# Performance work log

Measured on AMD Instinct MI355X. Metric: run time of the kernel, lower is better.

## Reference

```python
import jax, jax.numpy as jnp
import numpy as np

B, NO, NM, NV, E = 16, 512, 128, 64, 256
H, DK, MS, FF = 16, 16, 8, 512
TRANS_MAX = 100.0


def _ln(x):
    m = x.mean(-1, keepdims=True)
    v = ((x - m) ** 2).mean(-1, keepdims=True)
    return (x - m) * jax.lax.rsqrt(v + 1e-5)


def _inv_norm(x):
    # 1 - minmax-normalize over the whole per-batch matrix
    mn = x.min(axis=(1, 2), keepdims=True)
    mx = x.max(axis=(1, 2), keepdims=True)
    return 1.0 - (x - mn) / (mx - mn)


def _adjacency(proc_time, trans_time, MVpair_trans, mask_dyn, mask_ma):
    # masked copy of proc_time
    A_proc = jnp.where(mask_dyn, proc_time, 0.0)
    # keep only the per-row minimum nonzero entry (min_ProcTime_elements)
    nz = jnp.where(A_proc == 0.0, jnp.inf, A_proc)
    mn = nz.min(axis=2, keepdims=True)
    keep = (A_proc == mn) & (A_proc != 0.0)
    A_proc = A_proc * keep.astype(proc_time.dtype)
    A_proc_norm = (A_proc > 0.0).astype(proc_time.dtype)
    # machine-machine masks
    mask2 = mask_ma[:, None, :] & mask_ma[:, :, None]  # [B, nm, nm]
    A_procing = (~mask2).astype(proc_time.dtype)
    A_off = _inv_norm(MVpair_trans)
    tt = jnp.where(mask2, trans_time, TRANS_MAX + 1.0)
    A_on = _inv_norm(tt)
    return A_proc_norm, A_procing, A_off, A_on


def _block(row, col, cost, Wq, Wk, Wv, Wo, mW1, mb1, mW2, mb2, fW1, fb1, fW2, fb2):
    # MatNet-style mixed-score multi-head attention encoding block
    Bb, R, _ = row.shape
    C = col.shape[1]
    q = (row @ Wq).reshape(Bb, R, H, DK).transpose(0, 2, 1, 3)  # bhrd
    k = (col @ Wk).reshape(Bb, C, H, DK).transpose(0, 2, 1, 3)  # bhcd
    v = (col @ Wv).reshape(Bb, C, H, DK).transpose(0, 2, 1, 3)
    dot = jnp.einsum('bhrd,bhcd->bhrc', q, k) / jnp.sqrt(jnp.asarray(DK, row.dtype))
    two = jnp.stack([dot, jnp.broadcast_to(cost[:, None], dot.shape)], axis=-1)  # [B,H,R,C,2]
    hmix = jax.nn.relu(jnp.einsum('bhrct,hts->bhrcs', two, mW1) + mb1[None, :, None, None, :])
    score = jnp.einsum('bhrcs,hso->bhrco', hmix, mW2)[..., 0] + mb2[:, 0][None, :, None, None]
    attn = jax.nn.softmax(score, axis=-1)
    ctx = jnp.einsum('bhrc,bhcd->bhrd', attn, v).transpose(0, 2, 1, 3).reshape(Bb, R, H * DK)
    out1 = _ln(row + ctx @ Wo)
    ffn = jax.nn.relu(out1 @ fW1 + fb1) @ fW2 + fb2
    return _ln(out1 + ffn)


def setup_inputs() -> dict:
    key = jax.random.key(0)
    ks = jax.random.split(key, 24)

    def nrm(i, shape, s=0.05):
        return jax.random.normal(ks[i], shape, jnp.float32) * s

    return {
        'ope_emb': nrm(0, (B, NO, E), 1.0),
        'ma_emb': nrm(1, (B, NM, E), 1.0),
        'veh_emb': nrm(2, (B, NV, E), 1.0),
        'proc_time': jax.random.uniform(ks[3], (B, NO, NM), jnp.float32) * 20.0,
        'offload_trans_time': jax.random.uniform(ks[4], (B, NO, NV), jnp.float32) * TRANS_MAX,
        'trans_time': jax.random.uniform(ks[5], (B, NM, NM), jnp.float32) * TRANS_MAX,
        'MVpair_trans': jax.random.uniform(ks[6], (B, NV, NM), jnp.float32) * TRANS_MAX,
        'mask_dyn_ope_ma_adj': jax.random.bernoulli(ks[7], 0.3, (B, NO, NM)),
        'mask_ma': jax.random.bernoulli(ks[8], 0.7, (B, NM)),
        # stacked params for the 4 blocks: 0=ope, 1=veh, 2=ma1, 3=ma2
        'Wq': nrm(9, (4, E, H * DK)),
        'Wk': nrm(10, (4, E, H * DK)),
        'Wv': nrm(11, (4, E, H * DK)),
        'Wo': nrm(12, (4, H * DK, E)),
        'mixW1': nrm(13, (4, H, 2, MS), 0.3),
        'mixb1': jnp.zeros((4, H, MS), jnp.float32),
        'mixW2': nrm(14, (4, H, MS, 1), 0.3),
        'mixb2': jnp.zeros((4, H, 1), jnp.float32),
        'ffW1': nrm(15, (4, E, FF)),
        'ffb1': jnp.zeros((4, FF), jnp.float32),
        'ffW2': nrm(16, (4, FF, E)),
        'ffb2': jnp.zeros((4, E), jnp.float32),
        'maprojW': nrm(17, (2 * E, E)),
        'maprojb': jnp.zeros((E,), jnp.float32),
    }


def reference(ope_emb, ma_emb, veh_emb, proc_time, offload_trans_time, trans_time,
              MVpair_trans, mask_dyn_ope_ma_adj, mask_ma,
              Wq, Wk, Wv, Wo, mixW1, mixb1, mixW2, mixb2,
              ffW1, ffb1, ffW2, ffb2, maprojW, maprojb):
    A_proc_norm, A_procing, A_off, A_on = _adjacency(
        proc_time, trans_time, MVpair_trans, mask_dyn_ope_ma_adj, mask_ma)

    def blk(i, row, col, cost):
        return _block(row, col, cost, Wq[i], Wk[i], Wv[i], Wo[i],
                      mixW1[i], mixb1[i], mixW2[i], mixb2[i],
                      ffW1[i], ffb1[i], ffW2[i], ffb2[i])

    ope_out = blk(0, ope_emb, ma_emb, A_proc_norm)
    veh_out = blk(1, veh_emb, ma_emb, A_off)
    ma1 = blk(2, ma_emb, ma_emb, A_procing)
    ma2 = blk(3, ma_emb, ma_emb, A_on)
    ma_out = jnp.concatenate([ma1, ma2], axis=-1) @ maprojW + maprojb
    return (ope_out, ma_out, veh_out)
```

## Files before the change

kernel.cpp:

```cpp
#include <hip/hip_runtime.h>
#include <hip/hip_fp16.h>
#include <hip/hip_bf16.h>


typedef unsigned short u16;
typedef __attribute__((ext_vector_type(8))) short bf16x8;
typedef __attribute__((ext_vector_type(4))) float f32x4;
struct us4 { u16 x, y, z, w; };

__device__ __forceinline__ float bf2f(u16 u) {
  return __uint_as_float(((unsigned int)u) << 16);
}
__device__ __forceinline__ u16 f2bf(float f) {
  unsigned int x = __float_as_uint(f);
  x += 0x7FFFu + ((x >> 16) & 1u);
  return (u16)(x >> 16);
}
__device__ __forceinline__ __half2 h2max(__half2 a, __half2 b) {
  unsigned au = *(unsigned*)&a, bu = *(unsigned*)&b, ru;
  asm("v_pk_max_f16 %0, %1, %2" : "=v"(ru) : "v"(au), "v"(bu));
  return *(__half2*)&ru;
}

#define NBATCH 16
#define NOPE   512
#define NMA    128
#define NVEH   64
#define EDIM   256

struct PrepArgs {
  const float* ope; const float* ma; const float* veh;
  u16* ope_bf; u16* ma_bf; u16* veh_bf;
  const float* proc; const int* mask_dyn; float* A_proc;
  const float* mv; const float* trans; const int* mask_ma;
  unsigned int* mm;
};
struct TrArgs {
  const float* Wq; const float* Wk; const float* Wv; const float* Wo;
  const float* ffW1; const float* ffW2; const float* maproj;
  u16* WqT; u16* WkT; u16* WvT; u16* WoT; u16* ffW1T; u16* ffW2T; u16* maprojT;
};
__global__ __launch_bounds__(256) void prep_a(PrepArgs a, TrArgs tr) {
  int blk = blockIdx.x, t = threadIdx.x;
  if (blk < 2816) {
    int i = blk * 256 + t;
    const float* s; u16* d; int j;
    if (i < 524288)      { s = a.ope; d = a.ope_bf; j = i; }
    else if (i < 655360) { s = a.ma;  d = a.ma_bf;  j = i - 524288; }
    else                 { s = a.veh; d = a.veh_bf; j = i - 655360; }
    float4 v = ((const float4*)s)[j];
    us4 o = { f2bf(v.x), f2bf(v.y), f2bf(v.z), f2bf(v.w) };
    ((us4*)d)[j] = o;
    return;
  }
  if (blk < 6912) {
    int local = blk - 2816;
    int row = local * 2 + (t >> 7);
    int lane = t & 127;
    size_t idx = (size_t)row * NMA + lane;
    float av = a.mask_dyn[idx] ? a.proc[idx] : 0.0f;
    float cand = (av != 0.0f) ? av : 1.0e30f;
    __shared__ float red[256];
    red[t] = cand;
    __syncthreads();
    for (int s = 64; s > 0; s >>= 1) {
      if (lane < s) red[t] = fminf(red[t], red[t + s]);
      __syncthreads();
    }
    float mn = red[t & 128];
    a.A_proc[idx] = (av != 0.0f && av == mn) ? 1.0f : 0.0f;
    return;
  }
  if (blk < 7104) {
    __shared__ float smn[256], smx[256];
    float mn = 1.0e30f, mx = -1.0e30f;
    int mmIdx;
    if (blk < 6976) {
      int local = blk - 6912;
      int b = local >> 2, chunk = local & 3;
      const float* xb = a.mv + (size_t)b * 8192 + chunk * 2048;
#pragma unroll
      for (int r = 0; r < 8; r++) {
        float v = xb[r * 256 + t];
        mn = fminf(mn, v);
        mx = fmaxf(mx, v);
      }
      mmIdx = b;
    } else {
      int local = blk - 6976;
      int b = local >> 3, chunk = local & 7;
      __shared__ unsigned char mrow[NMA];
      if (t < NMA) mrow[t] = (unsigned char)(a.mask_ma[(size_t)b * NMA + t] != 0);
      __syncthreads();
      const float* tb = a.trans + (size_t)b * 16384 + chunk * 2048;
      int rbase = chunk * 16;
#pragma unroll
      for (int r = 0; r < 8; r++) {
        int off = r * 256 + t;
        int row = rbase + (off >> 7), col = off & 127;
        bool m2 = mrow[row] && mrow[col];
        float tt = m2 ? tb[off] : 101.0f;
        mn = fminf(mn, tt);
        mx = fmaxf(mx, tt);
      }
      mmIdx = 16 + b;
    }
    smn[t] = mn; smx[t] = mx;
    __syncthreads();
    for (int s = 128; s > 0; s >>= 1) {
      if (t < s) {
        smn[t] = fminf(smn[t], smn[t + s]);
        smx[t] = fmaxf(smx[t], smx[t + s]);
      }
      __syncthreads();
    }
    if (t == 0) {
      atomicMin(&a.mm[mmIdx], __float_as_uint(smn[0]));
      atomicMax(&a.mm[32 + mmIdx], __float_as_uint(smx[0]));
    }
    return;
  }
  {
    int b2 = blk - 7104;
    const float* src; u16* dst; int Kd, Nd, tile;
    if (b2 < 1024) {
      int w = b2 >> 8, i = (b2 >> 6) & 3; tile = b2 & 63;
      const float* sw = (w == 0 ? tr.Wq : w == 1 ? tr.Wk : w == 2 ? tr.Wv : tr.Wo);
      u16* dw = (w == 0 ? tr.WqT : w == 1 ? tr.WkT : w == 2 ? tr.WvT : tr.WoT);
      src = sw + (size_t)i * 65536; dst = dw + (size_t)i * 65536;
      Kd = 256; Nd = 256;
    } else if (b2 < 1536) {
      int z = (b2 - 1024) >> 7; tile = (b2 - 1024) & 127;
      src = tr.ffW1 + (size_t)z * 131072; dst = tr.ffW1T + (size_t)z * 131072;
      Kd = 256; Nd = 512;
    } else {
      int z = (b2 - 1536) >> 7; tile = (b2 - 1536) & 127;
      if (z < 4) { src = tr.ffW2 + (size_t)z * 131072; dst = tr.ffW2T + (size_t)z * 131072; }
      else       { src = tr.maproj; dst = tr.maprojT; }
      Kd = 512; Nd = 256;
    }
    int nx = Nd >> 5;
    int k0 = (tile / nx) * 32, n0 = (tile % nx) * 32;
    __shared__ float tl[32][33];
    int tx = t & 31, ty = t >> 5;
#pragma unroll
    for (int r = 0; r < 4; r++)
      tl[ty + r * 8][tx] = src[(size_t)(k0 + ty + r * 8) * Nd + n0 + tx];
    __syncthreads();
#pragma unroll
    for (int r = 0; r < 4; r++)
      dst[(size_t)(n0 + ty + r * 8) * Kd + k0 + tx] = f2bf(tl[tx][ty + r * 8]);
  }
}

struct PB {
  const float* mv; const float* trans; const int* mask_ma;
  const unsigned int* mm; float* A_offb; float* a_on; float* a_pcing;
};
__device__ __forceinline__ void prep_b_body(const PB& p, int blk, int t) {
  if (blk < 512) {
    int b = blk >> 5, off = (blk & 31) * 256 + t;
    float lo = __uint_as_float(p.mm[b]);
    float inv = 1.0f / (__uint_as_float(p.mm[32 + b]) - lo);
    size_t idx = (size_t)b * 8192 + off;
    p.A_offb[idx] = 1.0f - (p.mv[idx] - lo) * inv;
    return;
  }
  int local = blk - 512;
  int b = local >> 6, off = (local & 63) * 256 + t;
  int row = off >> 7, col = off & 127;
  bool m2 = (p.mask_ma[(size_t)b * NMA + row] != 0) &&
            (p.mask_ma[(size_t)b * NMA + col] != 0);
  size_t idx = (size_t)b * 16384 + off;
  float tt = m2 ? p.trans[idx] : 101.0f;
  float lo = __uint_as_float(p.mm[16 + b]);
  float inv = 1.0f / (__uint_as_float(p.mm[48 + b]) - lo);
  p.a_on[idx] = 1.0f - (tt - lo) * inv;
  p.a_pcing[idx] = m2 ? 0.0f : 1.0f;
}

struct GG {
  const u16* A; const u16* WT; const float* bias; u16* C;
  int M, N, K, epi, wgStart, cshift, mode;
};
struct GGArgs { GG g[12]; PB pb; int n; int nGemmWG; };

__global__ __launch_bounds__(256) void gemm_grouped(GGArgs args) {
  int wg = blockIdx.x;
  if (wg >= args.nGemmWG) {
    prep_b_body(args.pb, wg - args.nGemmWG, threadIdx.x);
    return;
  }
  int gi = 0;
  for (int i = 1; i < args.n; i++)
    if (wg >= args.g[i].wgStart) gi = i;
  GG gg = args.g[gi];
  int lwg = wg - gg.wgStart;
  int bx = lwg & ((1 << gg.cshift) - 1);
  int by = lwg >> gg.cshift;
  int N = gg.N, K = gg.K;

  __shared__ u16 As[128][40];
  __shared__ u16 Bs[128][40];
  int tid = threadIdx.x;
  int lane = tid & 63, wid = tid >> 6;
  int wr = (wid >> 1) * 64, wc = (wid & 1) * 64;
  int m16 = lane & 15, quad = lane >> 4;
  int rb = by * 128, cb = bx * 128;
  int srow = tid >> 2;
  int schunk = (tid & 3) * 8;

  f32x4 acc[4][4];
#pragma unroll
  for (int i = 0; i < 4; i++)
#pragma unroll
    for (int j = 0; j < 4; j++) acc[i][j] = (f32x4){0.f, 0.f, 0.f, 0.f};

  for (int k0 = 0; k0 < K; k0 += 32) {
    uint4 va0 = *(const uint4*)(gg.A + (size_t)(rb + srow) * K + k0 + schunk);
    uint4 va1 = *(const uint4*)(gg.A + (size_t)(rb + 64 + srow) * K + k0 + schunk);
    uint4 vb0 = *(const uint4*)(gg.WT + (size_t)(cb + srow) * K + k0 + schunk);
    uint4 vb1 = *(const uint4*)(gg.WT + (size_t)(cb + 64 + srow) * K + k0 + schunk);
    __syncthreads();
    *(uint4*)&As[srow][schunk] = va0;
    *(uint4*)&As[64 + srow][schunk] = va1;
    *(uint4*)&Bs[srow][schunk] = vb0;
    *(uint4*)&Bs[64 + srow][schunk] = vb1;
    __syncthreads();
    bf16x8 af[4], bfr[4];
#pragma unroll
    for (int i = 0; i < 4; i++)
      af[i] = *(const bf16x8*)&As[wr + i * 16 + m16][quad * 8];
#pragma unroll
    for (int j = 0; j < 4; j++)
      bfr[j] = *(const bf16x8*)&Bs[wc + j * 16 + m16][quad * 8];
#pragma unroll
    for (int i = 0; i < 4; i++)
#pragma unroll
      for (int j = 0; j < 4; j++)
        acc[i][j] = __builtin_amdgcn_mfma_f32_16x16x32_bf16(
            af[i], bfr[j], acc[i][j], 0, 0, 0);
  }

#pragma unroll
  for (int i = 0; i < 4; i++) {
#pragma unroll
    for (int j = 0; j < 4; j++) {
      int col = cb + wc + j * 16 + m16;
      float bv = (gg.epi >= 1) ? gg.bias[col] : 0.0f;
      if (gg.mode == 3) {
        int row0 = rb + wr + i * 16 + quad * 4;
        int b = row0 >> 7, c0 = row0 & 127;
        us4 o = { f2bf(acc[i][j][0]), f2bf(acc[i][j][1]),
                  f2bf(acc[i][j][2]), f2bf(acc[i][j][3]) };
        *(us4*)(gg.C + (size_t)b * 32768 + (size_t)col * 128 + c0) = o;
      } else {
#pragma unroll
        for (int r = 0; r < 4; r++) {
          int row = rb + wr + i * 16 + quad * 4 + r;
          float v = acc[i][j][r] + bv;
          if (gg.epi == 2) v = fmaxf(v, 0.0f);
          size_t off;
          if (gg.mode == 0) {
            off = (size_t)row * N + col;
          } else if (gg.mode == 1) {
            off = ((size_t)(row >> 4)) * 4096 + (size_t)(col >> 4) * 256 +
                  (size_t)(row & 15) * 16 + (col & 15);
          } else {
            off = ((size_t)(row >> 7)) * 32768 + (size_t)(col >> 4) * 2048 +
                  (size_t)(row & 127) * 16 + (col & 15);
          }
          gg.C[off] = f2bf(v);
        }
      }
    }
  }
}

__global__ __launch_bounds__(256) void gemm_mfma_f32(
    const u16* __restrict__ A, const u16* __restrict__ WT,
    const float* __restrict__ bias, float* __restrict__ C,
    int M, int N, int K) {
  __shared__ u16 As[64][40];
  __shared__ u16 Bs[64][40];
  int tid = threadIdx.x;
  int lane = tid & 63, wid = tid >> 6;
  int wr = (wid >> 1) * 32, wc = (wid & 1) * 32;
  int m16 = lane & 15, quad = lane >> 4;
  int rb = blockIdx.y * 64, cb = blockIdx.x * 64;
  int srow = tid >> 2;
  int schunk = (tid & 3) * 8;
  f32x4 acc[2][2];
#pragma unroll
  for (int i = 0; i < 2; i++)
#pragma unroll
    for (int j = 0; j < 2; j++) acc[i][j] = (f32x4){0.f, 0.f, 0.f, 0.f};
  for (int k0 = 0; k0 < K; k0 += 32) {
    uint4 va = *(const uint4*)(A + (size_t)(rb + srow) * K + k0 + schunk);
    uint4 vb = *(const uint4*)(WT + (size_t)(cb + srow) * K + k0 + schunk);
    __syncthreads();
    *(uint4*)&As[srow][schunk] = va;
    *(uint4*)&Bs[srow][schunk] = vb;
    __syncthreads();
    bf16x8 af[2], bfr[2];
#pragma unroll
    for (int i = 0; i < 2; i++)
      af[i] = *(const bf16x8*)&As[wr + i * 16 + m16][quad * 8];
#pragma unroll
    for (int j = 0; j < 2; j++)
      bfr[j] = *(const bf16x8*)&Bs[wc + j * 16 + m16][quad * 8];
#pragma unroll
    for (int i = 0; i < 2; i++)
#pragma unroll
      for (int j = 0; j < 2; j++)
        acc[i][j] = __builtin_amdgcn_mfma_f32_16x16x32_bf16(
            af[i], bfr[j], acc[i][j], 0, 0, 0);
  }
#pragma unroll
  for (int i = 0; i < 2; i++)
#pragma unroll
    for (int j = 0; j < 2; j++) {
      int col = cb + wc + j * 16 + m16;
      float bv = bias[col];
#pragma unroll
      for (int r = 0; r < 4; r++) {
        int row = rb + wr + i * 16 + quad * 4 + r;
        C[(size_t)row * N + col] = acc[i][j][r] + bv;
      }
    }
}

struct AG {
  const u16* q; const u16* k; const u16* vT; const float* cost; u16* ctx;
  const float* w1; const float* b1; const float* w2; const float* b2;
  int R, wgStart;
};
struct AGArgs { AG g[4]; };

#define CSTRIDE 134

__global__ __launch_bounds__(256) void attn_grouped(AGArgs args) {
  int blk = blockIdx.x;
  int gi = 0;
#pragma unroll
  for (int i = 1; i < 4; i++)
    if (blk >= args.g[i].wgStart) gi = i;
  AG gg = args.g[gi];
  int local = blk - gg.wgStart;

  int t = threadIdx.x;
  int wave = t >> 6, lane = t & 63;
  int quad = lane >> 4, l16 = lane & 15;
  int j = local & 15;
  int b = (j & 7) * 2 + (j >> 3);
  int hgrp = (local >> 4) & 1;
  int tile = local >> 5;
  int m0 = b * gg.R + tile * 16;

  __shared__ __half costs_h[16 * CSTRIDE];
  __shared__ u16 pbuf[4][16 * 136];

  const float* cp = gg.cost + (size_t)m0 * 128;
  for (int i = t; i < 2048; i += 256)
    costs_h[(i >> 7) * CSTRIDE + (i & 127)] = __float2half(cp[i]);
  __syncthreads();

  const bf16x8 zerof = (bf16x8){0, 0, 0, 0, 0, 0, 0, 0};
  const f32x4 zacc = (f32x4){0.f, 0.f, 0.f, 0.f};
  const __half2 zh = __float2half2_rn(0.0f);
  u16* pb = pbuf[wave];
  const u16* qtile = gg.q + ((size_t)(m0 >> 4)) * 4096;
  const u16* kb    = gg.k + (size_t)b * 32768;

#pragma unroll
  for (int hh = 0; hh < 2; hh++) {
    int h = hgrp * 8 + wave * 2 + hh;

    __half2 w10h[8], w11h[8], b1h[8], w2h[8];
#pragma unroll
    for (int s = 0; s < 8; s++) {
      w10h[s] = __float2half2_rn(gg.w1[h * 16 + s] * 0.25f);
      w11h[s] = __float2half2_rn(gg.w1[h * 16 + 8 + s]);
      b1h[s]  = __float2half2_rn(gg.b1[h * 8 + s]);
      w2h[s]  = __float2half2_rn(gg.w2[h * 8 + s]);
    }
    float wb2v = gg.b2[h];

    bf16x8 bq = zerof;
    if (quad < 2)
      bq = *(const bf16x8*)(qtile + (size_t)h * 256 + l16 * 16 + quad * 8);
    f32x4 st[8];
    __builtin_amdgcn_s_setprio(1);
#pragma unroll
    for (int ct = 0; ct < 8; ct++) {
      bf16x8 ak = zerof;
      if (quad < 2)
        ak = *(const bf16x8*)(kb + (size_t)h * 2048 + (ct * 16 + l16) * 16 +
                              quad * 8);
      st[ct] = __builtin_amdgcn_mfma_f32_16x16x32_bf16(ak, bq, zacc, 0, 0, 0);
    }
    __builtin_amdgcn_s_setprio(0);

#pragma unroll
    for (int ct = 0; ct < 8; ct++) {
#pragma unroll
      for (int p = 0; p < 2; p++) {
        __half2 d2 = __float22half2_rn(
            make_float2(st[ct][p * 2], st[ct][p * 2 + 1]));
        __half2 c2 = *(const __half2*)&costs_h[l16 * CSTRIDE + ct * 16 +
                                               quad * 4 + p * 2];
        __half2 s2 = zh;
#pragma unroll
        for (int s = 0; s < 8; s++) {
          __half2 hm = __hfma2(d2, w10h[s], __hfma2(c2, w11h[s], b1h[s]));
          hm = h2max(hm, zh);
          s2 = __hfma2(hm, w2h[s], s2);
        }
        float2 sf = __half22float2(s2);
        st[ct][p * 2]     = sf.x + wb2v;
        st[ct][p * 2 + 1] = sf.y + wb2v;
      }
    }

    float mx = -1.0e30f;
#pragma unroll
    for (int ct = 0; ct < 8; ct++)
#pragma unroll
      for (int rg = 0; rg < 4; rg++) mx = fmaxf(mx, st[ct][rg]);
    mx = fmaxf(mx, __shfl_xor(mx, 16, 64));
    mx = fmaxf(mx, __shfl_xor(mx, 32, 64));
    float sum = 0.0f;
#pragma unroll
    for (int ct = 0; ct < 8; ct++)
#pragma unroll
      for (int rg = 0; rg < 4; rg++) {
        float e = __expf(st[ct][rg] - mx);
        st[ct][rg] = e;
        sum += e;
      }
    sum += __shfl_xor(sum, 16, 64);
    sum += __shfl_xor(sum, 32, 64);
    float inv = 1.0f / sum;

#pragma unroll
    for (int ct = 0; ct < 8; ct++) {
#pragma unroll
      for (int p = 0; p < 2; p++) {
        __hip_bfloat162 pk = __float22bfloat162_rn(
            make_float2(st[ct][p * 2] * inv, st[ct][p * 2 + 1] * inv));
        *(unsigned int*)&pb[l16 * 136 + ct * 16 + quad * 4 + p * 2] =
            *(unsigned int*)&pk;
      }
    }

    f32x4 cacc = zacc;
    __builtin_amdgcn_s_setprio(1);
#pragma unroll
    for (int ks = 0; ks < 4; ks++) {
      bf16x8 ap = *(const bf16x8*)&pb[l16 * 136 + ks * 32 + quad * 8];
      bf16x8 bv = *(const bf16x8*)(gg.vT + (size_t)b * 32768 +
                                   (size_t)(h * 16 + l16) * 128 + ks * 32 +
                                   quad * 8);
      cacc = __builtin_amdgcn_mfma_f32_16x16x32_bf16(ap, bv, cacc, 0, 0, 0);
    }
    __builtin_amdgcn_s_setprio(0);

#pragma unroll
    for (int rg = 0; rg < 4; rg++)
      gg.ctx[(size_t)(m0 + quad * 4 + rg) * 256 + h * 16 + l16] =
          f2bf(cacc[rg]);
  }
}

struct FTArgs {
  const u16* ctx;
  const float* rope; const float* rveh; const float* rma;
  const u16* WoT; const u16* W1T; const u16* W2T;
  const float* ffb1; const float* ffb2;
  float* outOpe; float* outVeh; u16* maCat;
};

__global__ __launch_bounds__(256, 4) void fused_tail(FTArgs a) {
  int rb = blockIdx.x * 16;
  int gi = (rb < 8192) ? 0 : (rb < 9216) ? 1 : (rb < 11264) ? 2 : 3;
  const u16* WoT = a.WoT + (size_t)gi * 65536;
  const u16* W1T = a.W1T + (size_t)gi * 131072;
  const u16* W2T = a.W2T + (size_t)gi * 131072;
  const float* b1p = a.ffb1 + gi * 512;
  const float* b2p = a.ffb2 + gi * 256;
  const float* resid; int lr0;
  if (gi == 0)      { resid = a.rope; lr0 = rb; }
  else if (gi == 1) { resid = a.rveh; lr0 = rb - 8192; }
  else if (gi == 2) { resid = a.rma;  lr0 = rb - 9216; }
  else              { resid = a.rma;  lr0 = rb - 11264; }

  __shared__ u16 O1[16][264];
  __shared__ u16 Fs[16][264];
  __shared__ float redS[16][4];
  __shared__ float redQ[16][4];

  int tid = threadIdx.x;
  int lane = tid & 63, wid = tid >> 6;
  int m16 = lane & 15, quad = lane >> 4;
  int wc = wid * 64;

  f32x4 acc1[4];
#pragma unroll
  for (int j = 0; j < 4; j++) acc1[j] = (f32x4){0.f, 0.f, 0.f, 0.f};
  {
    const u16* ap = a.ctx + (size_t)(rb + m16) * 256;
    bf16x8 afc, afn, bfc[4], bfn[4];
    afc = *(const bf16x8*)(ap + quad * 8);
#pragma unroll
    for (int j = 0; j < 4; j++)
      bfc[j] = *(const bf16x8*)(WoT + (size_t)(wc + j * 16 + m16) * 256 + quad * 8);
#pragma unroll
    for (int k0 = 0; k0 < 256; k0 += 32) {
      if (k0 + 32 < 256) {
        afn = *(const bf16x8*)(ap + k0 + 32 + quad * 8);
#pragma unroll
        for (int j = 0; j < 4; j++)
          bfn[j] = *(const bf16x8*)(WoT + (size_t)(wc + j * 16 + m16) * 256 +
                                    k0 + 32 + quad * 8);
      }
#pragma unroll
      for (int j = 0; j < 4; j++)
        acc1[j] = __builtin_amdgcn_mfma_f32_16x16x32_bf16(
            afc, bfc[j], acc1[j], 0, 0, 0);
      afc = afn;
#pragma unroll
      for (int j = 0; j < 4; j++) bfc[j] = bfn[j];
    }
  }

#pragma unroll
  for (int j = 0; j < 4; j++) {
    int colj = wc + j * 16 + m16;
#pragma unroll
    for (int r = 0; r < 4; r++)
      acc1[j][r] += resid[(size_t)(lr0 + quad * 4 + r) * 256 + colj];
  }
#pragma unroll
  for (int r = 0; r < 4; r++) {
    float s = acc1[0][r] + acc1[1][r] + acc1[2][r] + acc1[3][r];
    float q = acc1[0][r] * acc1[0][r] + acc1[1][r] * acc1[1][r] +
              acc1[2][r] * acc1[2][r] + acc1[3][r] * acc1[3][r];
#pragma unroll
    for (int d = 1; d < 16; d <<= 1) {
      s += __shfl_xor(s, d, 64);
      q += __shfl_xor(q, d, 64);
    }
    if (m16 == 0) {
      redS[quad * 4 + r][wid] = s;
      redQ[quad * 4 + r][wid] = q;
    }
  }
  __syncthreads();
#pragma unroll
  for (int r = 0; r < 4; r++) {
    int row = quad * 4 + r;
    float s = redS[row][0] + redS[row][1] + redS[row][2] + redS[row][3];
    float q = redQ[row][0] + redQ[row][1] + redQ[row][2] + redQ[row][3];
    float mean = s * (1.0f / 256.0f);
    float var = q * (1.0f / 256.0f) - mean * mean;
    float rs = rsqrtf(fmaxf(var, 0.0f) + 1e-5f);
#pragma unroll
    for (int j = 0; j < 4; j++)
      O1[row][wc + j * 16 + m16] = f2bf((acc1[j][r] - mean) * rs);
  }
  __syncthreads();

  f32x4 acc3[4];
#pragma unroll
  for (int j = 0; j < 4; j++) acc3[j] = (f32x4){0.f, 0.f, 0.f, 0.f};

  for (int h = 0; h < 2; h++) {
    const u16* W1h = W1T + (size_t)h * 65536;
    f32x4 acc2[4];
#pragma unroll
    for (int j = 0; j < 4; j++) acc2[j] = (f32x4){0.f, 0.f, 0.f, 0.f};
    {
      bf16x8 bfc[4], bfn[4];
#pragma unroll
      for (int j = 0; j < 4; j++)
        bfc[j] = *(const bf16x8*)(W1h + (size_t)(wc + j * 16 + m16) * 256 +
                                  quad * 8);
#pragma unroll
      for (int k0 = 0; k0 < 256; k0 += 32) {
        if (k0 + 32 < 256) {
#pragma unroll
          for (int j = 0; j < 4; j++)
            bfn[j] = *(const bf16x8*)(W1h + (size_t)(wc + j * 16 + m16) * 256 +
                                      k0 + 32 + quad * 8);
        }
        bf16x8 af = *(const bf16x8*)&O1[m16][k0 + quad * 8];
#pragma unroll
        for (int j = 0; j < 4; j++)
          acc2[j] = __builtin_amdgcn_mfma_f32_16x16x32_bf16(
              af, bfc[j], acc2[j], 0, 0, 0);
#pragma unroll
        for (int j = 0; j < 4; j++) bfc[j] = bfn[j];
      }
    }
#pragma unroll
    for (int j = 0; j < 4; j++) {
      int coll = wc + j * 16 + m16;
      float bv = b1p[h * 256 + coll];
#pragma unroll
      for (int r = 0; r < 4; r++)
        Fs[quad * 4 + r][coll] = f2bf(fmaxf(acc2[j][r] + bv, 0.0f));
    }
    __syncthreads();
    {
      bf16x8 bfc[4], bfn[4];
#pragma unroll
      for (int j = 0; j < 4; j++)
        bfc[j] = *(const bf16x8*)(W2T + (size_t)(wc + j * 16 + m16) * 512 +
                                  h * 256 + quad * 8);
#pragma unroll
      for (int k0 = 0; k0 < 256; k0 += 32) {
        if (k0 + 32 < 256) {
#pragma unroll
          for (int j = 0; j < 4; j++)
            bfn[j] = *(const bf16x8*)(W2T + (size_t)(wc + j * 16 + m16) * 512 +
                                      h * 256 + k0 + 32 + quad * 8);
        }
        bf16x8 af = *(const bf16x8*)&Fs[m16][k0 + quad * 8];
#pragma unroll
        for (int j = 0; j < 4; j++)
          acc3[j] = __builtin_amdgcn_mfma_f32_16x16x32_bf16(
              af, bfc[j], acc3[j], 0, 0, 0);
#pragma unroll
        for (int j = 0; j < 4; j++) bfc[j] = bfn[j];
      }
    }
    __syncthreads();
  }

#pragma unroll
  for (int j = 0; j < 4; j++) {
    int colj = wc + j * 16 + m16;
    float bv = b2p[colj];
#pragma unroll
    for (int r = 0; r < 4; r++)
      acc3[j][r] += bv + bf2f(O1[quad * 4 + r][colj]);
  }
#pragma unroll
  for (int r = 0; r < 4; r++) {
    float s = acc3[0][r] + acc3[1][r] + acc3[2][r] + acc3[3][r];
    float q = acc3[0][r] * acc3[0][r] + acc3[1][r] * acc3[1][r] +
              acc3[2][r] * acc3[2][r] + acc3[3][r] * acc3[3][r];
#pragma unroll
    for (int d = 1; d < 16; d <<= 1) {
      s += __shfl_xor(s, d, 64);
      q += __shfl_xor(q, d, 64);
    }
    if (m16 == 0) {
      redS[quad * 4 + r][wid] = s;
      redQ[quad * 4 + r][wid] = q;
    }
  }
  __syncthreads();
#pragma unroll
  for (int r = 0; r < 4; r++) {
    int row = quad * 4 + r;
    float s = redS[row][0] + redS[row][1] + redS[row][2] + redS[row][3];
    float q = redQ[row][0] + redQ[row][1] + redQ[row][2] + redQ[row][3];
    float mean = s * (1.0f / 256.0f);
    float var = q * (1.0f / 256.0f) - mean * mean;
    float rs = rsqrtf(fmaxf(var, 0.0f) + 1e-5f);
#pragma unroll
    for (int j = 0; j < 4; j++) {
      int colj = wc + j * 16 + m16;
      float y = (acc3[j][r] - mean) * rs;
      if (gi == 0)
        a.outOpe[(size_t)(lr0 + row) * 256 + colj] = y;
      else if (gi == 1)
        a.outVeh[(size_t)(lr0 + row) * 256 + colj] = y;
      else if (gi == 2)
        a.maCat[(size_t)(lr0 + row) * 512 + colj] = f2bf(y);
      else
        a.maCat[(size_t)(lr0 + row) * 512 + 256 + colj] = f2bf(y);
    }
  }
}

extern "C" void kernel_launch(void* const* d_in, const int* in_sizes, int n_in,
                              void* d_out, int out_size, void* d_ws, size_t ws_size,
                              hipStream_t stream) {
  const float* ope   = (const float*)d_in[0];
  const float* ma    = (const float*)d_in[1];
  const float* veh   = (const float*)d_in[2];
  const float* proc  = (const float*)d_in[3];
  const float* trans = (const float*)d_in[5];
  const float* mv    = (const float*)d_in[6];
  const int* mask_dyn = (const int*)d_in[7];
  const int* mask_ma  = (const int*)d_in[8];
  const float* Wq = (const float*)d_in[9];
  const float* Wk = (const float*)d_in[10];
  const float* Wv = (const float*)d_in[11];
  const float* Wo = (const float*)d_in[12];
  const float* mixW1 = (const float*)d_in[13];
  const float* mixb1 = (const float*)d_in[14];
  const float* mixW2 = (const float*)d_in[15];
  const float* mixb2 = (const float*)d_in[16];
  const float* ffW1 = (const float*)d_in[17];
  const float* ffb1 = (const float*)d_in[18];
  const float* ffW2 = (const float*)d_in[19];
  const float* ffb2 = (const float*)d_in[20];
  const float* maprojW = (const float*)d_in[21];
  const float* maprojb = (const float*)d_in[22];
  float* out = (float*)d_out;
  char* ws = (char*)d_ws;

  const int OFF[4] = {0, 8192, 9216, 11264};
  const int MS4[4] = {8192, 1024, 2048, 2048};

  const size_t MB = 1 << 20;
  float* A_proc  = (float*)(ws + 0);
  float* A_offb  = (float*)(ws + 4 * MB);
  float* A_pcing = (float*)(ws + 4 * MB + MB / 2);
  float* A_on    = (float*)(ws + 5 * MB + MB / 2);
  u16* ope_bf  = (u16*)(ws + 6 * MB + MB / 2);
  u16* ma_bf   = (u16*)(ws + 10 * MB + MB / 2);
  u16* veh_bf  = (u16*)(ws + 11 * MB + MB / 2);
  u16* WqT     = (u16*)(ws + 12 * MB);
  u16* WkT     = (u16*)(ws + 12 * MB + MB / 2);
  u16* WvT     = (u16*)(ws + 13 * MB);
  u16* WoT     = (u16*)(ws + 13 * MB + MB / 2);
  u16* ffW1T   = (u16*)(ws + 14 * MB);
  u16* ffW2T   = (u16*)(ws + 15 * MB);
  u16* maprojT = (u16*)(ws + 16 * MB);
  u16* q_all   = (u16*)(ws + 16 * MB + MB / 2);
  u16* k_all   = (u16*)(ws + 23 * MB);
  u16* vT_all  = (u16*)(ws + 31 * MB);
  u16* ctx_all = (u16*)(ws + 35 * MB);
  u16* maCat   = (u16*)(ws + 67 * MB + MB / 2);
  unsigned int* mmbuf = (unsigned int*)(ws + 70 * MB);

  hipMemsetAsync(mmbuf, 0x7F, 128, stream);
  hipMemsetAsync((char*)mmbuf + 128, 0x00, 128, stream);

  {
    PrepArgs pa = {ope, ma, veh, ope_bf, ma_bf, veh_bf,
                   proc, mask_dyn, A_proc, mv, trans, mask_ma, mmbuf};
    TrArgs ta = {Wq, Wk, Wv, Wo, ffW1, ffW2, maprojW,
                 WqT, WkT, WvT, WoT, ffW1T, ffW2T, maprojT};
    prep_a<<<9280, 256, 0, stream>>>(pa, ta);
  }

  const size_t MA_OUT  = (size_t)NBATCH * NOPE * EDIM;
  const size_t VEH_OUT = MA_OUT + (size_t)NBATCH * NMA * EDIM;

  const u16* rowbf[4] = {ope_bf, veh_bf, ma_bf, ma_bf};
  const float* costp[4] = {A_proc, A_offb, A_pcing, A_on};
  PB pb = {mv, trans, mask_ma, mmbuf, A_offb, A_on, A_pcing};

  {
    GGArgs ga; ga.n = 12; ga.pb = pb;
    int wg = 0;
    for (int i = 0; i < 4; i++) {
      ga.g[i] = {rowbf[i], WqT + (size_t)i * 65536, nullptr,
                 q_all + (size_t)OFF[i] * 256, MS4[i], 256, 256, 0, wg, 1, 1};
      wg += (MS4[i] / 128) * 2;
    }
    for (int i = 0; i < 4; i++) {
      ga.g[4 + i] = {ma_bf, WkT + (size_t)i * 65536, nullptr,
                     k_all + (size_t)i * 524288, 2048, 256, 256, 0, wg, 1, 2};
      wg += 32;
    }
    for (int i = 0; i < 4; i++) {
      ga.g[8 + i] = {ma_bf, WvT + (size_t)i * 65536, nullptr,
                     vT_all + (size_t)i * 524288, 2048, 256, 256, 0, wg, 1, 3};
      wg += 32;
    }
    ga.nGemmWG = wg;
    gemm_grouped<<<wg + 1536, 256, 0, stream>>>(ga);
  }

  {
    AGArgs aa;
    int wg = 0;
    const int R4[4] = {NOPE, NVEH, NMA, NMA};
    for (int i = 0; i < 4; i++) {
      aa.g[i] = {q_all + (size_t)OFF[i] * 256, k_all + (size_t)i * 524288,
                 vT_all + (size_t)i * 524288, costp[i],
                 ctx_all + (size_t)OFF[i] * 256,
                 mixW1 + (size_t)i * 256, mixb1 + (size_t)i * 128,
                 mixW2 + (size_t)i * 128, mixb2 + (size_t)i * 16,
                 R4[i], wg};
      wg += MS4[i] / 8;
    }
    attn_grouped<<<wg, 256, 0, stream>>>(aa);
  }

  {
    FTArgs fa = {ctx_all, ope, veh, ma, WoT, ffW1T, ffW2T, ffb1, ffb2,
                 out, out + VEH_OUT, maCat};
    fused_tail<<<832, 256, 0, stream>>>(fa);
  }

  gemm_mfma_f32<<<dim3(4, 32), 256, 0, stream>>>(maCat, maprojT, maprojb,
      out + MA_OUT, 2048, 256, 512);
}
```

Baseline: 265.3 us.

## Run fused tail with one wavefront per row block covering all columns

```diff
diff --git a/kernel.cpp b/kernel.cpp
--- a/kernel.cpp
+++ b/kernel.cpp
@@ -480,7 +480,7 @@
   float* outOpe; float* outVeh; u16* maCat;
 };
 
-__global__ __launch_bounds__(256, 4) void fused_tail(FTArgs a) {
+__global__ __launch_bounds__(64, 1) void fused_tail(FTArgs a) {
   int rb = blockIdx.x * 16;
   int gi = (rb < 8192) ? 0 : (rb < 9216) ? 1 : (rb < 11264) ? 2 : 3;
   const u16* WoT = a.WoT + (size_t)gi * 65536;
@@ -496,150 +496,107 @@
 
   __shared__ u16 O1[16][264];
   __shared__ u16 Fs[16][264];
-  __shared__ float redS[16][4];
-  __shared__ float redQ[16][4];
-
-  int tid = threadIdx.x;
-  int lane = tid & 63, wid = tid >> 6;
+
+  int lane = threadIdx.x & 63;
   int m16 = lane & 15, quad = lane >> 4;
-  int wc = wid * 64;
-
-  f32x4 acc1[4];
-#pragma unroll
-  for (int j = 0; j < 4; j++) acc1[j] = (f32x4){0.f, 0.f, 0.f, 0.f};
+
+  f32x4 acc1[16];
+#pragma unroll
+  for (int j = 0; j < 16; j++) acc1[j] = (f32x4){0.f, 0.f, 0.f, 0.f};
   {
     const u16* ap = a.ctx + (size_t)(rb + m16) * 256;
-    bf16x8 afc, afn, bfc[4], bfn[4];
-    afc = *(const bf16x8*)(ap + quad * 8);
-#pragma unroll
-    for (int j = 0; j < 4; j++)
-      bfc[j] = *(const bf16x8*)(WoT + (size_t)(wc + j * 16 + m16) * 256 + quad * 8);
 #pragma unroll
     for (int k0 = 0; k0 < 256; k0 += 32) {
-      if (k0 + 32 < 256) {
-        afn = *(const bf16x8*)(ap + k0 + 32 + quad * 8);
-#pragma unroll
-        for (int j = 0; j < 4; j++)
-          bfn[j] = *(const bf16x8*)(WoT + (size_t)(wc + j * 16 + m16) * 256 +
-                                    k0 + 32 + quad * 8);
-      }
-#pragma unroll
-      for (int j = 0; j < 4; j++)
+      bf16x8 af = *(const bf16x8*)(ap + k0 + quad * 8);
+      bf16x8 bf[16];
+#pragma unroll
+      for (int j = 0; j < 16; j++)
+        bf[j] = *(const bf16x8*)(WoT + (size_t)(j * 16 + m16) * 256 +
+                                 k0 + quad * 8);
+#pragma unroll
+      for (int j = 0; j < 16; j++)
         acc1[j] = __builtin_amdgcn_mfma_f32_16x16x32_bf16(
-            afc, bfc[j], acc1[j], 0, 0, 0);
-      afc = afn;
-#pragma unroll
-      for (int j = 0; j < 4; j++) bfc[j] = bfn[j];
-    }
-  }
-
-#pragma unroll
-  for (int j = 0; j < 4; j++) {
-    int colj = wc + j * 16 + m16;
+            af, bf[j], acc1[j], 0, 0, 0);
+    }
+  }
+
+#pragma unroll
+  for (int j = 0; j < 16; j++) {
+    int colj = j * 16 + m16;
 #pragma unroll
     for (int r = 0; r < 4; r++)
       acc1[j][r] += resid[(size_t)(lr0 + quad * 4 + r) * 256 + colj];
   }
 #pragma unroll
   for (int r = 0; r < 4; r++) {
-    float s = acc1[0][r] + acc1[1][r] + acc1[2][r] + acc1[3][r];
-    float q = acc1[0][r] * acc1[0][r] + acc1[1][r] * acc1[1][r] +
-              acc1[2][r] * acc1[2][r] + acc1[3][r] * acc1[3][r];
+    float s = 0.f, q = 0.f;
+#pragma unroll
+    for (int j = 0; j < 16; j++) {
+      s += acc1[j][r];
+      q += acc1[j][r] * acc1[j][r];
+    }
 #pragma unroll
     for (int d = 1; d < 16; d <<= 1) {
       s += __shfl_xor(s, d, 64);
       q += __shfl_xor(q, d, 64);
     }
-    if (m16 == 0) {
-      redS[quad * 4 + r][wid] = s;
-      redQ[quad * 4 + r][wid] = q;
-    }
-  }
-  __syncthreads();
-#pragma unroll
-  for (int r = 0; r < 4; r++) {
-    int row = quad * 4 + r;
-    float s = redS[row][0] + redS[row][1] + redS[row][2] + redS[row][3];
-    float q = redQ[row][0] + redQ[row][1] + redQ[row][2] + redQ[row][3];
     float mean = s * (1.0f / 256.0f);
     float var = q * (1.0f / 256.0f) - mean * mean;
     float rs = rsqrtf(fmaxf(var, 0.0f) + 1e-5f);
-#pragma unroll
-    for (int j = 0; j < 4; j++)
-      O1[row][wc + j * 16 + m16] = f2bf((acc1[j][r] - mean) * rs);
-  }
-  __syncthreads();
-
-  f32x4 acc3[4];
-#pragma unroll
-  for (int j = 0; j < 4; j++) acc3[j] = (f32x4){0.f, 0.f, 0.f, 0.f};
+    int row = quad * 4 + r;
+#pragma unroll
+    for (int j = 0; j < 16; j++)
+      O1[row][j * 16 + m16] = f2bf((acc1[j][r] - mean) * rs);
+  }
+
+  f32x4 acc3[16];
+#pragma unroll
+  for (int j = 0; j < 16; j++) acc3[j] = (f32x4){0.f, 0.f, 0.f, 0.f};
 
   for (int h = 0; h < 2; h++) {
     const u16* W1h = W1T + (size_t)h * 65536;
-    f32x4 acc2[4];
-#pragma unroll
-    for (int j = 0; j < 4; j++) acc2[j] = (f32x4){0.f, 0.f, 0.f, 0.f};
-    {
-      bf16x8 bfc[4], bfn[4];
-#pragma unroll
-      for (int j = 0; j < 4; j++)
-        bfc[j] = *(const bf16x8*)(W1h + (size_t)(wc + j * 16 + m16) * 256 +
-                                  quad * 8);
-#pragma unroll
-      for (int k0 = 0; k0 < 256; k0 += 32) {
-        if (k0 + 32 < 256) {
-#pragma unroll
-          for (int j = 0; j < 4; j++)
-            bfn[j] = *(const bf16x8*)(W1h + (size_t)(wc + j * 16 + m16) * 256 +
-                                      k0 + 32 + quad * 8);
-        }
-        bf16x8 af = *(const bf16x8*)&O1[m16][k0 + quad * 8];
-#pragma unroll
-        for (int j = 0; j < 4; j++)
-          acc2[j] = __builtin_amdgcn_mfma_f32_16x16x32_bf16(
-              af, bfc[j], acc2[j], 0, 0, 0);
-#pragma unroll
-        for (int j = 0; j < 4; j++) bfc[j] = bfn[j];
-      }
-    }
-#pragma unroll
-    for (int j = 0; j < 4; j++) {
-      int coll = wc + j * 16 + m16;
+    f32x4 acc2[16];
+#pragma unroll
+    for (int j = 0; j < 16; j++) acc2[j] = (f32x4){0.f, 0.f, 0.f, 0.f};
+#pragma unroll
+    for (int k0 = 0; k0 < 256; k0 += 32) {
+      bf16x8 af = *(const bf16x8*)&O1[m16][k0 + quad * 8];
+      bf16x8 bf[16];
+#pragma unroll
+      for (int j = 0; j < 16; j++)
+        bf[j] = *(const bf16x8*)(W1h + (size_t)(j * 16 + m16) * 256 +
+                                 k0 + quad * 8);
+#pragma unroll
+      for (int j = 0; j < 16; j++)
+        acc2[j] = __builtin_amdgcn_mfma_f32_16x16x32_bf16(
+            af, bf[j], acc2[j], 0, 0, 0);
+    }
+#pragma unroll
+    for (int j = 0; j < 16; j++) {
+      int coll = j * 16 + m16;
       float bv = b1p[h * 256 + coll];
 #pragma unroll
       for (int r = 0; r < 4; r++)
         Fs[quad * 4 + r][coll] = f2bf(fmaxf(acc2[j][r] + bv, 0.0f));
     }
-    __syncthreads();
-    {
-      bf16x8 bfc[4], bfn[4];
-#pragma unroll
-      for (int j = 0; j < 4; j++)
-        bfc[j] = *(const bf16x8*)(W2T + (size_t)(wc + j * 16 + m16) * 512 +
-                                  h * 256 + quad * 8);
-#pragma unroll
-      for (int k0 = 0; k0 < 256; k0 += 32) {
-        if (k0 + 32 < 256) {
-#pragma unroll
-          for (int j = 0; j < 4; j++)
-            bfn[j] = *(const bf16x8*)(W2T + (size_t)(wc + j * 16 + m16) * 512 +
-                                      h * 256 + k0 + 32 + quad * 8);
-        }
-        bf16x8 af = *(const bf16x8*)&Fs[m16][k0 + quad * 8];
-#pragma unroll
-        for (int j = 0; j < 4; j++)
-          acc3[j] = __builtin_amdgcn_mfma_f32_16x16x32_bf16(
-              af, bfc[j], acc3[j], 0, 0, 0);
-#pragma unroll
-        for (int j = 0; j < 4; j++) bfc[j] = bfn[j];
-      }
-    }
-    __syncthreads();
-  }
-
-#pragma unroll
-  for (int j = 0; j < 4; j++) {
-    int colj = wc + j * 16 + m16;
+#pragma unroll
+    for (int k0 = 0; k0 < 256; k0 += 32) {
+      bf16x8 af = *(const bf16x8*)&Fs[m16][k0 + quad * 8];
+      bf16x8 bf[16];
+#pragma unroll
+      for (int j = 0; j < 16; j++)
+        bf[j] = *(const bf16x8*)(W2T + (size_t)(j * 16 + m16) * 512 +
+                                 h * 256 + k0 + quad * 8);
+#pragma unroll
+      for (int j = 0; j < 16; j++)
+        acc3[j] = __builtin_amdgcn_mfma_f32_16x16x32_bf16(
+            af, bf[j], acc3[j], 0, 0, 0);
+    }
+  }
+
+#pragma unroll
+  for (int j = 0; j < 16; j++) {
+    int colj = j * 16 + m16;
     float bv = b2p[colj];
 #pragma unroll
     for (int r = 0; r < 4; r++)
@@ -647,31 +604,24 @@
   }
 #pragma unroll
   for (int r = 0; r < 4; r++) {
-    float s = acc3[0][r] + acc3[1][r] + acc3[2][r] + acc3[3][r];
-    float q = acc3[0][r] * acc3[0][r] + acc3[1][r] * acc3[1][r] +
-              acc3[2][r] * acc3[2][r] + acc3[3][r] * acc3[3][r];
+    float s = 0.f, q = 0.f;
+#pragma unroll
+    for (int j = 0; j < 16; j++) {
+      s += acc3[j][r];
+      q += acc3[j][r] * acc3[j][r];
+    }
 #pragma unroll
     for (int d = 1; d < 16; d <<= 1) {
       s += __shfl_xor(s, d, 64);
       q += __shfl_xor(q, d, 64);
     }
-    if (m16 == 0) {
-      redS[quad * 4 + r][wid] = s;
-      redQ[quad * 4 + r][wid] = q;
-    }
-  }
-  __syncthreads();
-#pragma unroll
-  for (int r = 0; r < 4; r++) {
-    int row = quad * 4 + r;
-    float s = redS[row][0] + redS[row][1] + redS[row][2] + redS[row][3];
-    float q = redQ[row][0] + redQ[row][1] + redQ[row][2] + redQ[row][3];
     float mean = s * (1.0f / 256.0f);
     float var = q * (1.0f / 256.0f) - mean * mean;
     float rs = rsqrtf(fmaxf(var, 0.0f) + 1e-5f);
-#pragma unroll
-    for (int j = 0; j < 4; j++) {
-      int colj = wc + j * 16 + m16;
+    int row = quad * 4 + r;
+#pragma unroll
+    for (int j = 0; j < 16; j++) {
+      int colj = j * 16 + m16;
       float y = (acc3[j][r] - mean) * rs;
       if (gi == 0)
         a.outOpe[(size_t)(lr0 + row) * 256 + colj] = y;
@@ -797,7 +747,7 @@
   {
     FTArgs fa = {ctx_all, ope, veh, ma, WoT, ffW1T, ffW2T, ffb1, ffb2,
                  out, out + VEH_OUT, maCat};
-    fused_tail<<<832, 256, 0, stream>>>(fa);
+    fused_tail<<<832, 64, 0, stream>>>(fa);
   }
 
   gemm_mfma_f32<<<dim3(4, 32), 256, 0, stream>>>(maCat, maprojT, maprojb,
```

Result: slower. 273.7 us (+3.2%).
